# Kernel optimization log

Measured on AMD Instinct MI355X. Metric: run time of the kernel, lower is better.

Reference implementation:

```python
import jax, jax.numpy as jnp
import numpy as np

D_MODEL = 1024
N_HEADS = 16
D_HEAD = D_MODEL // N_HEADS
EPS = 1e-5
ROPE_BASE = 10000.0


def layer_norm(x, w, b=None):
    mu = jnp.mean(x, axis=-1, keepdims=True)
    var = jnp.var(x, axis=-1, keepdims=True)
    y = (x - mu) * jax.lax.rsqrt(var + EPS) * w
    return y + b if b is not None else y


def rope_cos_sin(seq_len, d_head, dtype):
    inv_freq = 1.0 / (ROPE_BASE ** (jnp.arange(0, d_head, 2, dtype=jnp.float32) / d_head))
    t = jnp.arange(seq_len, dtype=jnp.float32)
    freqs = jnp.einsum('l,f->lf', t, inv_freq)          # [L, d_head/2]
    emb = jnp.concatenate([freqs, freqs], axis=-1)       # [L, d_head]
    return jnp.cos(emb).astype(dtype), jnp.sin(emb).astype(dtype)


def rotate_half(x):
    x1, x2 = jnp.split(x, 2, axis=-1)
    return jnp.concatenate([-x2, x1], axis=-1)


def apply_rotary(x, cos, sin):
    # x: [B, L, H, Dh]; cos/sin: [L, Dh]
    c = cos[None, :, None, :]
    s = sin[None, :, None, :]
    return x * c + rotate_half(x) * s


def setup_inputs() -> dict:
    key = jax.random.key(0)
    ks = jax.random.split(key, 8)
    B, L, D = 2, 2048, D_MODEL
    x = jax.random.normal(ks[0], (B, L, D), dtype=jnp.float32)
    seq_id = jnp.sort(jax.random.randint(ks[1], (B, L), 0, 4), axis=-1).astype(jnp.int32)
    scale = 1.0 / np.sqrt(D)
    return {
        'x': x,
        'seq_id': seq_id,
        'ln1_w': jnp.ones((D,), jnp.float32),
        'ln1_b': jnp.zeros((D,), jnp.float32),
        'w_qkv': jax.random.normal(ks[2], (D, 3 * D), jnp.float32) * scale,
        'q_ln_w': jnp.ones((D,), jnp.float32),
        'k_ln_w': jnp.ones((D,), jnp.float32),
        'w_out': jax.random.normal(ks[3], (D, D), jnp.float32) * scale,
    }


def reference(x, seq_id, ln1_w, ln1_b, w_qkv, q_ln_w, k_ln_w, w_out):
    B, L, D = x.shape
    h = layer_norm(x, ln1_w, ln1_b)
    qkv = h @ w_qkv                                    # [B, L, 3D]
    q, k, v = jnp.split(qkv, 3, axis=-1)
    q = layer_norm(q, q_ln_w)                          # qk-LN over full d_model, no bias
    k = layer_norm(k, k_ln_w)
    q = q.reshape(B, L, N_HEADS, D_HEAD)
    k = k.reshape(B, L, N_HEADS, D_HEAD)
    v = v.reshape(B, L, N_HEADS, D_HEAD)
    cos, sin = rope_cos_sin(L, D_HEAD, x.dtype)
    q = apply_rotary(q, cos, sin)
    k = apply_rotary(k, cos, sin)
    scale = 1.0 / np.sqrt(D_HEAD)
    scores = jnp.einsum('bqhd,bkhd->bhqk', q, k) * scale   # [B, H, L, L]
    mask = (seq_id[:, :, None] == seq_id[:, None, :])[:, None, :, :]  # [B,1,L,L]
    scores = jnp.where(mask, scores, jnp.finfo(scores.dtype).min)
    probs = jax.nn.softmax(scores, axis=-1)
    ctx = jnp.einsum('bhqk,bkhd->bqhd', probs, v).reshape(B, L, D)
    return ctx @ w_out
```

## Files before the change

### kernel.cpp

```cpp
#include <hip/hip_runtime.h>
#include <hip/hip_bf16.h>
#include <cstdint>
#include <math.h>

#define LSEQ 2048
#define BATCH 2
#define NHEAD 16
#define DHEAD 64
#define DMODEL 1024
#define ROWS (BATCH*LSEQ)

typedef __bf16 bf16x8 __attribute__((ext_vector_type(8)));
typedef float f32x4 __attribute__((ext_vector_type(4)));
typedef unsigned short u16;

#define GLD(lds_base, src_g) \
  __builtin_amdgcn_global_load_lds((const __attribute__((address_space(1))) void*)(src_g), \
                                   (__attribute__((address_space(3))) void*)(lds_base), 16, 0, 0)
#define VM(n) asm volatile("s_waitcnt vmcnt(" #n ")" ::: "memory")

__device__ __forceinline__ u16 f2bf(float f) {
  unsigned int u = __float_as_uint(f);
  u += 0x7fffu + ((u >> 16) & 1u);
  return (u16)(u >> 16);
}
__device__ __forceinline__ float bf2f(u16 u) {
  return __uint_as_float(((unsigned)u) << 16);
}

__global__ void k_transpose_cvt(const float* __restrict__ in, u16* __restrict__ out, int R, int C) {
  __shared__ float tile[32][33];
  int c0 = blockIdx.x * 32, r0 = blockIdx.y * 32;
  int tx = threadIdx.x, ty = threadIdx.y;
#pragma unroll
  for (int i = 0; i < 32; i += 8)
    tile[ty + i][tx] = in[(size_t)(r0 + ty + i) * C + (c0 + tx)];
  __syncthreads();
#pragma unroll
  for (int i = 0; i < 32; i += 8)
    out[(size_t)(c0 + ty + i) * R + (r0 + tx)] = f2bf(tile[tx][ty + i]);
}

__global__ void k_transpose_u16(const u16* __restrict__ in, u16* __restrict__ out) {
  __shared__ u16 tile[32][33];
  int hd = blockIdx.z;
  int l0 = blockIdx.y * 32, d0 = blockIdx.x * 32;
  const u16* ip = in + (size_t)hd * LSEQ * DHEAD;
  u16* op = out + (size_t)hd * LSEQ * DHEAD;
  int tx = threadIdx.x, ty = threadIdx.y;
#pragma unroll
  for (int i = 0; i < 32; i += 8)
    tile[ty + i][tx] = ip[(size_t)(l0 + ty + i) * DHEAD + d0 + tx];
  __syncthreads();
#pragma unroll
  for (int i = 0; i < 32; i += 8)
    op[(size_t)(d0 + ty + i) * LSEQ + l0 + tx] = tile[tx][ty + i];
}

__global__ void k_rope_tables(float* __restrict__ cosb, float* __restrict__ sinb,
                              const int* __restrict__ seq, int* __restrict__ bnd) {
  if (blockIdx.x == 0 && threadIdx.x < BATCH * 5) {
    int b = threadIdx.x / 5, s = threadIdx.x % 5;
    const int* row = seq + b * LSEQ;
    int lo = 0, hi = LSEQ;
    while (lo < hi) { int mid = (lo + hi) >> 1; if (row[mid] < s) lo = mid + 1; else hi = mid; }
    bnd[b * 5 + s] = lo;
  }
  int idx = blockIdx.x * blockDim.x + threadIdx.x;
  if (idx >= LSEQ * 32) return;
  int l = idx >> 5, f = idx & 31;
  double inv = pow(10000.0, -(double)f / 32.0);
  float ang = (float)l * (float)inv;
  cosb[idx] = cosf(ang);
  sinb[idx] = sinf(ang);
}

__global__ __launch_bounds__(256) void k_ln1(const float* __restrict__ x, const float* __restrict__ w,
                                             const float* __restrict__ bias, u16* __restrict__ h) {
  int row = blockIdx.x, t = threadIdx.x;
  const float4 xv = ((const float4*)(x + (size_t)row * DMODEL))[t];
  float s = xv.x + xv.y + xv.z + xv.w;
  float s2 = xv.x * xv.x + xv.y * xv.y + xv.z * xv.z + xv.w * xv.w;
#pragma unroll
  for (int m2 = 1; m2 < 64; m2 <<= 1) { s += __shfl_xor(s, m2); s2 += __shfl_xor(s2, m2); }
  __shared__ float rb[2][4];
  int wv = t >> 6;
  if ((t & 63) == 0) { rb[0][wv] = s; rb[1][wv] = s2; }
  __syncthreads();
  s  = rb[0][0] + rb[0][1] + rb[0][2] + rb[0][3];
  s2 = rb[1][0] + rb[1][1] + rb[1][2] + rb[1][3];
  float mu = s * (1.0f / DMODEL);
  float rs = rsqrtf(s2 * (1.0f / DMODEL) - mu * mu + 1e-5f);
  const float4 wv4 = ((const float4*)w)[t];
  const float4 bv4 = ((const float4*)bias)[t];
  ushort4 o;
  o.x = f2bf((xv.x - mu) * rs * wv4.x + bv4.x);
  o.y = f2bf((xv.y - mu) * rs * wv4.y + bv4.y);
  o.z = f2bf((xv.z - mu) * rs * wv4.z + bv4.z);
  o.w = f2bf((xv.w - mu) * rs * wv4.w + bv4.w);
  ((ushort4*)(h + (size_t)row * DMODEL))[t] = o;
}

template<int OUTMODE>
__global__ __launch_bounds__(512, 2) void k_gemm256(const u16* __restrict__ A, const u16* __restrict__ B,
                                                    void* __restrict__ Cv, int M, int N, int K) {
  __shared__ __align__(16) u16 As[2][256 * 64];
  __shared__ __align__(16) u16 Bs[2][192 * 64];
  const int t = threadIdx.x, lane = t & 63, w = t >> 6;
  const int wr = w >> 2, wc = w & 3;
  const int nbx = N / 192;
  const int nwg = nbx * (M >> 8);
  const int cpx = nwg >> 3;
  const int bid = blockIdx.x;
  const int sw = (bid & 7) * cpx + (bid >> 3);
  const int m0 = (sw / nbx) * 256, n0 = (sw % nbx) * 192;
  const int NT = K >> 6;
  const int cg16 = (lane >> 4) * 16;

  f32x4 acc[8][3] = {};
  bf16x8 af_[4][2], bf_[3][2];
  const u16* Ap = A + (size_t)m0 * K;
  const u16* Bp = B + (size_t)n0 * K;
  const int rr0 = t >> 3;
  const int sz = ((t & 7) * 8) ^ ((rr0 & 7) << 3);
  const u16* pA[4] = { Ap + (size_t)rr0 * K + sz,
                       Ap + (size_t)(rr0 + 64) * K + sz,
                       Ap + (size_t)(rr0 + 128) * K + sz,
                       Ap + (size_t)(rr0 + 192) * K + sz };
  const u16* pB[3] = { Bp + (size_t)rr0 * K + sz,
                       Bp + (size_t)(rr0 + 64) * K + sz,
                       Bp + (size_t)(rr0 + 128) * K + sz };

#define SA2(b, h, EO) do { \
    GLD((char*)As + (b)*32768 + (h)*16384 + w*1024,        pA[(h)*2]     + (EO)); \
    GLD((char*)As + (b)*32768 + (h)*16384 + 8192 + w*1024, pA[(h)*2 + 1] + (EO)); \
  } while (0)
#define SB3(b, EO) do { \
    GLD((char*)Bs + (b)*24576 +         w*1024, pB[0] + (EO)); \
    GLD((char*)Bs + (b)*24576 +  8192 + w*1024, pB[1] + (EO)); \
    GLD((char*)Bs + (b)*24576 + 16384 + w*1024, pB[2] + (EO)); \
  } while (0)

#define READ_AF(asb, mh) do { \
    _Pragma("unroll") for (int i2 = 0; i2 < 4; i2++) { \
      const int rowA = (((mh)*4 + i2)*2 + wr)*16 + (lane & 15); \
      const int sA = (rowA & 7) << 4; \
      _Pragma("unroll") for (int kk = 0; kk < 2; kk++) \
        af_[i2][kk] = *(const bf16x8*)((const char*)(asb) + (rowA & 127)*128 + ((kk*64 + cg16) ^ sA)); \
    } } while (0)
#define READ_BF(bsb) do { \
    _Pragma("unroll") for (int j2 = 0; j2 < 3; j2++) { \
      const int rowB = (j2*4 + wc)*16 + (lane & 15); \
      const int sB = (rowB & 7) << 4; \
      _Pragma("unroll") for (int kk = 0; kk < 2; kk++) \
        bf_[j2][kk] = *(const bf16x8*)((const char*)(bsb) + rowB*128 + ((kk*64 + cg16) ^ sB)); \
    } } while (0)
#define MFMA24(mh) do { \
    _Pragma("unroll") for (int kk = 0; kk < 2; kk++) \
      _Pragma("unroll") for (int i2 = 0; i2 < 4; i2++) \
        _Pragma("unroll") for (int j2 = 0; j2 < 3; j2++) \
          acc[(mh)*4+i2][j2] = __builtin_amdgcn_mfma_f32_16x16x32_bf16( \
              af_[i2][kk], bf_[j2][kk], acc[(mh)*4+i2][j2], 0, 0, 0); \
  } while (0)

  SA2(0, 0, 0); SA2(0, 1, 0); SB3(0, 0);
  SA2(1, 0, 64);
  VM(2);
  __builtin_amdgcn_s_barrier();

  const char* a0  = (const char*)As;
  const char* a0h = a0 + 16384;
  const char* a1  = a0 + 32768;
  const char* a1h = a0 + 49152;
  const char* b0  = (const char*)Bs;
  const char* b1  = b0 + 24576;
  const int NIT = NT >> 1;
  for (int i = 0; i < NIT; i++) {
    const bool lst = (i == NIT - 1);
    READ_AF(a0, 0); READ_BF(b0);
    SA2(1, 1, 64); SB3(1, 64);
    __builtin_amdgcn_s_barrier();
    asm volatile("s_waitcnt lgkmcnt(0)" ::: "memory");
    __builtin_amdgcn_s_setprio(1); MFMA24(0); __builtin_amdgcn_s_setprio(0);
    __builtin_amdgcn_s_barrier();
    READ_AF(a0h, 1);
    if (!lst) SA2(0, 0, 128);
    __builtin_amdgcn_s_barrier();
    asm volatile("s_waitcnt lgkmcnt(0)" ::: "memory");
    __builtin_amdgcn_s_setprio(1); MFMA24(1); __builtin_amdgcn_s_setprio(0);
    if (lst) VM(0); else VM(2);
    __builtin_amdgcn_s_barrier();
    READ_AF(a1, 0); READ_BF(b1);
    if (!lst) { SA2(0, 1, 128); SB3(0, 128); }
    __builtin_amdgcn_s_barrier();
    asm volatile("s_waitcnt lgkmcnt(0)" ::: "memory");
    __builtin_amdgcn_s_setprio(1); MFMA24(0); __builtin_amdgcn_s_setprio(0);
    __builtin_amdgcn_s_barrier();
    READ_AF(a1h, 1);
    if (!lst) SA2(1, 0, 192);
    __builtin_amdgcn_s_barrier();
    asm volatile("s_waitcnt lgkmcnt(0)" ::: "memory");
    __builtin_amdgcn_s_setprio(1); MFMA24(1); __builtin_amdgcn_s_setprio(0);
    if (!lst) VM(2);
    __builtin_amdgcn_s_barrier();
    pA[0] += 128; pA[1] += 128; pA[2] += 128; pA[3] += 128;
    pB[0] += 128; pB[1] += 128; pB[2] += 128;
  }
#undef MFMA24
#undef READ_BF
#undef READ_AF
#undef SA2
#undef SB3

  const int cr = (lane >> 4) * 4, cc = lane & 15;
#pragma unroll
  for (int fi = 0; fi < 8; fi++)
#pragma unroll
    for (int fj = 0; fj < 3; fj++) {
      const size_t roff = (size_t)(m0 + (fi * 2 + wr) * 16 + cr) * N + (n0 + (fj * 4 + wc) * 16 + cc);
      if (OUTMODE == 0) {
        float* Cp = (float*)Cv + roff;
#pragma unroll
        for (int r = 0; r < 4; r++) Cp[(size_t)r * N] = acc[fi][fj][r];
      } else {
        u16* Cp = (u16*)Cv + roff;
#pragma unroll
        for (int r = 0; r < 4; r++) Cp[(size_t)r * N] = f2bf(acc[fi][fj][r]);
      }
    }
}

template<int OUTMODE>
__global__ __launch_bounds__(256) void k_gemm_bt(const u16* __restrict__ A, const u16* __restrict__ B,
                                                 void* __restrict__ Cv, int M, int N, int K) {
  __shared__ __align__(16) u16 As[2][128 * 64];
  __shared__ __align__(16) u16 Bs[2][128 * 64];
  const int t = threadIdx.x;
  const int lane = t & 63, w = t >> 6;
  const int nbx = N >> 7;
  const int nwg = nbx * (M >> 7);
  const int cpx = nwg >> 3;
  const int bid = blockIdx.x;
  const int sw = (bid & 7) * cpx + (bid >> 3);
  const int m0 = (sw / nbx) * 128, n0 = (sw % nbx) * 128;
  const int wm = (w >> 1) * 64, wn = (w & 1) * 64;
  const int NT = K >> 6;
  f32x4 acc[4][4] = {};
  const u16* Ap = A + (size_t)m0 * K;
  const u16* Bp = B + (size_t)n0 * K;
  const int cr0 = lane >> 3, cs = lane & 7;

#define GSTAGE(bb, kt_) do { \
    _Pragma("unroll") \
    for (int s2 = 0; s2 < 4; s2++) { \
      int ch = w * 4 + s2; \
      int row = ch * 8 + cr0; \
      int cb = cs ^ (row & 7); \
      GLD((char*)As[bb] + ch * 1024, Ap + (size_t)row * K + (kt_) * 64 + cb * 8); \
      GLD((char*)Bs[bb] + ch * 1024, Bp + (size_t)row * K + (kt_) * 64 + cb * 8); \
    } } while (0)

  GSTAGE(0, 0);
  VM(0);
  __builtin_amdgcn_s_barrier();
  int cur = 0;
  for (int kt = 0; kt < NT; kt++) {
    if (kt + 1 < NT) GSTAGE(cur ^ 1, kt + 1);
    const u16* asb = As[cur];
    const u16* bsb = Bs[cur];
#pragma unroll
    for (int kk = 0; kk < 2; kk++) {
      bf16x8 af[4], bfr[4];
#pragma unroll
      for (int i = 0; i < 4; i++) {
        int rowa = wm + i * 16 + (lane & 15);
        af[i] = *(const bf16x8*)((const char*)asb + rowa * 128 + ((kk * 64 + (lane >> 4) * 16) ^ ((rowa & 7) << 4)));
        int rowb = wn + i * 16 + (lane & 15);
        bfr[i] = *(const bf16x8*)((const char*)bsb + rowb * 128 + ((kk * 64 + (lane >> 4) * 16) ^ ((rowb & 7) << 4)));
      }
#pragma unroll
      for (int mf = 0; mf < 4; mf++)
#pragma unroll
        for (int nf = 0; nf < 4; nf++)
          acc[mf][nf] = __builtin_amdgcn_mfma_f32_16x16x32_bf16(af[mf], bfr[nf], acc[mf][nf], 0, 0, 0);
    }
    VM(0);
    __builtin_amdgcn_s_barrier();
    cur ^= 1;
  }
#undef GSTAGE
  const int cr = (lane >> 4) * 4, cc = lane & 15;
#pragma unroll
  for (int mf = 0; mf < 4; mf++)
#pragma unroll
    for (int nf = 0; nf < 4; nf++) {
      if (OUTMODE == 0) {
        float* Cp = (float*)Cv + (size_t)(m0 + wm + mf * 16 + cr) * N + (n0 + wn + nf * 16 + cc);
#pragma unroll
        for (int r = 0; r < 4; r++) Cp[(size_t)r * N] = acc[mf][nf][r];
      } else {
        u16* Cp = (u16*)Cv + (size_t)(m0 + wm + mf * 16 + cr) * N + (n0 + wn + nf * 16 + cc);
#pragma unroll
        for (int r = 0; r < 4; r++) Cp[(size_t)r * N] = f2bf(acc[mf][nf][r]);
      }
    }
}

__global__ __launch_bounds__(256) void k_qk_ln_rope(const u16* __restrict__ qkv,
                                                    const float* __restrict__ qw, const float* __restrict__ kw,
                                                    const float* __restrict__ cosb, const float* __restrict__ sinb,
                                                    u16* __restrict__ Q, u16* __restrict__ K, u16* __restrict__ V) {
  int row = blockIdx.x, t = threadIdx.x;
  int b = row >> 11, l = row & 2047;
  const u16* base = qkv + (size_t)row * 3072;
  ushort4 qu = ((const ushort4*)base)[t];
  ushort4 ku = ((const ushort4*)(base + 1024))[t];
  ushort4 vu = ((const ushort4*)(base + 2048))[t];
  float qx = bf2f(qu.x), qy = bf2f(qu.y), qz = bf2f(qu.z), qw_ = bf2f(qu.w);
  float kx = bf2f(ku.x), ky = bf2f(ku.y), kz = bf2f(ku.z), kw_ = bf2f(ku.w);
  float red[4];
  red[0] = qx + qy + qz + qw_;
  red[1] = qx * qx + qy * qy + qz * qz + qw_ * qw_;
  red[2] = kx + ky + kz + kw_;
  red[3] = kx * kx + ky * ky + kz * kz + kw_ * kw_;
#pragma unroll
  for (int i = 0; i < 4; i++)
#pragma unroll
    for (int m2 = 1; m2 < 64; m2 <<= 1) red[i] += __shfl_xor(red[i], m2);
  __shared__ float rb[4][4];
  int w = t >> 6;
  if ((t & 63) == 0) { rb[w][0] = red[0]; rb[w][1] = red[1]; rb[w][2] = red[2]; rb[w][3] = red[3]; }
  __syncthreads();
  float S1 = rb[0][0] + rb[1][0] + rb[2][0] + rb[3][0];
  float S2 = rb[0][1] + rb[1][1] + rb[2][1] + rb[3][1];
  float S3 = rb[0][2] + rb[1][2] + rb[2][2] + rb[3][2];
  float S4 = rb[0][3] + rb[1][3] + rb[2][3] + rb[3][3];
  float muq = S1 * (1.0f / DMODEL), rsq = rsqrtf(S2 * (1.0f / DMODEL) - muq * muq + 1e-5f);
  float muk = S3 * (1.0f / DMODEL), rsk = rsqrtf(S4 * (1.0f / DMODEL) - muk * muk + 1e-5f);
  __shared__ float qs[1024], ks[1024];
  float4 qwv = ((const float4*)qw)[t];
  float4 kwv = ((const float4*)kw)[t];
  qs[t * 4 + 0] = (qx - muq) * rsq * qwv.x;  ks[t * 4 + 0] = (kx - muk) * rsk * kwv.x;
  qs[t * 4 + 1] = (qy - muq) * rsq * qwv.y;  ks[t * 4 + 1] = (ky - muk) * rsk * kwv.y;
  qs[t * 4 + 2] = (qz - muq) * rsq * qwv.z;  ks[t * 4 + 2] = (kz - muk) * rsk * kwv.z;
  qs[t * 4 + 3] = (qw_ - muq) * rsq * qwv.w; ks[t * 4 + 3] = (kw_ - muk) * rsk * kwv.w;
  __syncthreads();
  int d0 = t * 4;
  int hh = d0 >> 6;
  union { ushort4 v4; u16 e[4]; } qo, ko;
#pragma unroll
  for (int i = 0; i < 4; i++) {
    int d = d0 + i, dd = d & 63, fr = dd & 31;
    float c = cosb[l * 32 + fr], s = sinb[l * 32 + fr];
    float q1 = qs[d], q2 = (dd < 32) ? -qs[d + 32] : qs[d - 32];
    float k1 = ks[d], k2 = (dd < 32) ? -ks[d + 32] : ks[d - 32];
    qo.e[i] = f2bf(q1 * c + q2 * s);
    ko.e[i] = f2bf(k1 * c + k2 * s);
  }
  size_t oidx = ((size_t)(b * NHEAD + hh) * LSEQ + l) * DHEAD + (d0 & 63);
  *(ushort4*)(Q + oidx) = qo.v4;
  *(ushort4*)(K + oidx) = ko.v4;
  *(ushort4*)(V + oidx) = vu;
}

__global__ __launch_bounds__(512) void k_attn(const u16* __restrict__ Q, const u16* __restrict__ Kb,
                                              const u16* __restrict__ VTb, const int* __restrict__ seq,
                                              const int* __restrict__ bnd, u16* __restrict__ ctx) {
  __shared__ __align__(16) u16 Ks[2][64 * 64];
  __shared__ __align__(16) u16 Vs[2][64 * 64];
  __shared__ __align__(16) u16 Pw[8][16 * 64];

  const int bid = blockIdx.x;
  const int sw = (bid & 7) * 64 + (bid >> 3);
  const int qt = sw & 15, h = (sw >> 4) & 15, b = sw >> 8;
  const int t = threadIdx.x, l = t & 63, w = t >> 6;
  const int c = l & 15, g = l >> 4;
  const int q0 = qt * 128;
  const size_t hoff = (size_t)(b * NHEAD + h) * LSEQ * DHEAD;
  const u16* Qg = Q + hoff;
  const u16* Kg = Kb + hoff;
  const u16* Vg = VTb + hoff;
  const int* seqb = seq + b * LSEQ;
  const int* bnd5 = bnd + b * 5;

  const int qw0 = q0 + w * 16;
  const int myq = qw0 + c;
  const int sq = seqb[myq];
  const int lo = bnd5[sq], hi = bnd5[sq + 1];
  const int wlo = bnd5[seqb[qw0]];
  const int whi = bnd5[seqb[qw0 + 15] + 1];
  int kbeg = bnd5[seqb[q0]] & ~63;
  int kend = (bnd5[seqb[q0 + 127] + 1] + 63) & ~63;
  if (kend > LSEQ) kend = LSEQ;

  bf16x8 qf[2];
  qf[0] = *(const bf16x8*)(Qg + (size_t)myq * 64 + g * 8);
  qf[1] = *(const bf16x8*)(Qg + (size_t)myq * 64 + 32 + g * 8);

  f32x4 acc[4] = {};
  float lsum = 0.f;

  const int rr = t >> 3;
  const int szk = ((t & 7) * 8) ^ ((rr & 7) << 3);
  const u16* pK = Kg + (size_t)rr * 64 + szk;
  const u16* pV = Vg + (size_t)rr * LSEQ + szk;

#define STAGE(bb, kt_) do { \
    GLD((char*)Ks[bb] + w * 1024, pK + (size_t)(kt_) * 64); \
    GLD((char*)Vs[bb] + w * 1024, pV + (kt_)); \
  } while (0)

  STAGE(0, kbeg);
  int cur = 0;
  for (int kt = kbeg; kt < kend; kt += 64) {
    const bool more = (kt + 64) < kend;
    if (more) STAGE(cur ^ 1, kt + 64);
    if (more) VM(2);
    else      VM(0);
    __builtin_amdgcn_s_barrier();
    __builtin_amdgcn_sched_barrier(0);
    if (kt < whi && kt + 64 > wlo) {
      const u16* ksb = Ks[cur];
      const u16* vsb = Vs[cur];
      f32x4 st[4] = {};
#pragma unroll
      for (int kk = 0; kk < 2; kk++) {
        bf16x8 kf[4];
#pragma unroll
        for (int i = 0; i < 4; i++) {
          int row = i * 16 + c;
          kf[i] = *(const bf16x8*)((const char*)ksb + row * 128 + ((kk * 64 + g * 16) ^ ((row & 7) << 4)));
        }
#pragma unroll
        for (int i = 0; i < 4; i++)
          st[i] = __builtin_amdgcn_mfma_f32_16x16x32_bf16(kf[i], qf[kk], st[i], 0, 0, 0);
      }
      const int kb0 = kt + g * 4;
#pragma unroll
      for (int i = 0; i < 4; i++) {
        float p[4];
#pragma unroll
        for (int r = 0; r < 4; r++) {
          int kglob = kb0 + i * 16 + r;
          bool ok = ((unsigned)(kglob - lo)) < ((unsigned)(hi - lo));
          float x = ok ? fmaf(st[i][r], 0.125f, -8.0f) : -1e30f;
          p[r] = __expf(x);
          lsum += p[r];
        }
        unsigned w0, w1;
        asm("v_cvt_pk_bf16_f32 %0, %1, %2" : "=v"(w0) : "v"(p[0]), "v"(p[1]));
        asm("v_cvt_pk_bf16_f32 %0, %1, %2" : "=v"(w1) : "v"(p[2]), "v"(p[3]));
        uint2 wp; wp.x = w0; wp.y = w1;
        *(uint2*)((char*)Pw[w] + c * 128 + ((i * 32 + g * 8) ^ ((c & 7) << 4))) = wp;
      }
#pragma unroll
      for (int kk = 0; kk < 2; kk++) {
        bf16x8 pa = *(const bf16x8*)((char*)Pw[w] + c * 128 + ((kk * 64 + g * 16) ^ ((c & 7) << 4)));
        bf16x8 vf[4];
#pragma unroll
        for (int df = 0; df < 4; df++) {
          int row = df * 16 + c;
          vf[df] = *(const bf16x8*)((const char*)vsb + row * 128 + ((kk * 64 + g * 16) ^ ((row & 7) << 4)));
        }
#pragma unroll
        for (int df = 0; df < 4; df++)
          acc[df] = __builtin_amdgcn_mfma_f32_16x16x32_bf16(pa, vf[df], acc[df], 0, 0, 0);
      }
    }
    __builtin_amdgcn_sched_barrier(0);
    __builtin_amdgcn_s_barrier();
    cur ^= 1;
  }
#undef STAGE

  lsum += __shfl_xor(lsum, 16);
  lsum += __shfl_xor(lsum, 32);
#pragma unroll
  for (int r = 0; r < 4; r++) {
    float lr = __shfl(lsum, g * 4 + r, 64);
    float rls = 1.0f / lr;
    int qrow = qw0 + g * 4 + r;
    u16* op = ctx + (size_t)(b * LSEQ + qrow) * DMODEL + h * 64 + c;
#pragma unroll
    for (int df = 0; df < 4; df++)
      op[df * 16] = f2bf(acc[df][r] * rls);
  }
}

extern "C" void kernel_launch(void* const* d_in, const int* in_sizes, int n_in,
                              void* d_out, int out_size, void* d_ws, size_t ws_size,
                              hipStream_t stream) {
  const float* x    = (const float*)d_in[0];
  const int*   seq  = (const int*)d_in[1];
  const float* ln1w = (const float*)d_in[2];
  const float* ln1b = (const float*)d_in[3];
  const float* wqkv = (const float*)d_in[4];
  const float* qlnw = (const float*)d_in[5];
  const float* klnw = (const float*)d_in[6];
  const float* wout = (const float*)d_in[7];
  float* out = (float*)d_out;

  char* p = (char*)d_ws;
  u16* wqkvT = (u16*)p;  p += (size_t)3072 * 1024 * 2;
  u16* woutT = (u16*)p;  p += (size_t)1024 * 1024 * 2;
  u16* hbuf  = (u16*)p;  p += (size_t)ROWS * DMODEL * 2;
  u16* Qb    = (u16*)p;  p += (size_t)ROWS * DMODEL * 2;
  u16* Kbuf  = (u16*)p;  p += (size_t)ROWS * DMODEL * 2;
  u16* Vbuf  = (u16*)p;  p += (size_t)ROWS * DMODEL * 2;
  u16* VTbuf = (u16*)p;  p += (size_t)ROWS * DMODEL * 2;
  u16* ctxb  = (u16*)p;  p += (size_t)ROWS * DMODEL * 2;
  float* cosb = (float*)p; p += (size_t)LSEQ * 32 * 4;
  float* sinb = (float*)p; p += (size_t)LSEQ * 32 * 4;
  int* bnd   = (int*)p;  p += 256;
  u16* qkv   = (u16*)p;  p += (size_t)ROWS * 3072 * 2;

  k_transpose_cvt<<<dim3(3072 / 32, 1024 / 32), dim3(32, 8), 0, stream>>>(wqkv, wqkvT, 1024, 3072);
  k_transpose_cvt<<<dim3(1024 / 32, 1024 / 32), dim3(32, 8), 0, stream>>>(wout, woutT, 1024, 1024);
  k_rope_tables<<<(LSEQ * 32) / 256, 256, 0, stream>>>(cosb, sinb, seq, bnd);
  k_ln1<<<ROWS, 256, 0, stream>>>(x, ln1w, ln1b, hbuf);
  k_gemm256<1><<<(ROWS / 256) * (3072 / 192), 512, 0, stream>>>(hbuf, wqkvT, (void*)qkv, ROWS, 3072, 1024);
  k_qk_ln_rope<<<ROWS, 256, 0, stream>>>(qkv, qlnw, klnw, cosb, sinb, Qb, Kbuf, Vbuf);
  k_transpose_u16<<<dim3(DHEAD / 32, LSEQ / 32, BATCH * NHEAD), dim3(32, 8), 0, stream>>>(Vbuf, VTbuf);
  k_attn<<<BATCH * NHEAD * (LSEQ / 128), 512, 0, stream>>>(Qb, Kbuf, VTbuf, seq, bnd, ctxb);
  k_gemm_bt<0><<<(ROWS / 128) * (1024 / 128), 256, 0, stream>>>(ctxb, woutT, (void*)out, ROWS, 1024, 1024);
}
```

Before: 123.3 us.

## Fuse prep kernels into one launch and halve QKV GEMM M-tile

Merges the weight transpose/convert, rope table, segment boundary and LN1 kernels into a single block-dispatched prep kernel, removing three launches and their serialization gaps. Separately, the QKV GEMM tile shrinks from 256x192 to 128x192 with occupancy hint raised to 4, doubling the workgroup count to 512 so more CUs are busy. Smaller M tiles increase B-operand reloads and lower per-block arithmetic intensity.

New measurement: 112.3 us. 8.9% less time.

```diff
diff --git a/kernel.cpp b/kernel.cpp
--- a/kernel.cpp
+++ b/kernel.cpp
@@ -26,19 +26,6 @@
 }
 __device__ __forceinline__ float bf2f(u16 u) {
   return __uint_as_float(((unsigned)u) << 16);
-}
-
-__global__ void k_transpose_cvt(const float* __restrict__ in, u16* __restrict__ out, int R, int C) {
-  __shared__ float tile[32][33];
-  int c0 = blockIdx.x * 32, r0 = blockIdx.y * 32;
-  int tx = threadIdx.x, ty = threadIdx.y;
-#pragma unroll
-  for (int i = 0; i < 32; i += 8)
-    tile[ty + i][tx] = in[(size_t)(r0 + ty + i) * C + (c0 + tx)];
-  __syncthreads();
-#pragma unroll
-  for (int i = 0; i < 32; i += 8)
-    out[(size_t)(c0 + ty + i) * R + (r0 + tx)] = f2bf(tile[tx][ty + i]);
 }
 
 __global__ void k_transpose_u16(const u16* __restrict__ in, u16* __restrict__ out) {
@@ -57,84 +44,99 @@
     op[(size_t)(d0 + ty + i) * LSEQ + l0 + tx] = tile[tx][ty + i];
 }
 
-__global__ void k_rope_tables(float* __restrict__ cosb, float* __restrict__ sinb,
-                              const int* __restrict__ seq, int* __restrict__ bnd) {
-  if (blockIdx.x == 0 && threadIdx.x < BATCH * 5) {
-    int b = threadIdx.x / 5, s = threadIdx.x % 5;
-    const int* row = seq + b * LSEQ;
-    int lo = 0, hi = LSEQ;
-    while (lo < hi) { int mid = (lo + hi) >> 1; if (row[mid] < s) lo = mid + 1; else hi = mid; }
-    bnd[b * 5 + s] = lo;
+__global__ __launch_bounds__(256) void k_prep(const float* __restrict__ x, const float* __restrict__ ln1w,
+                                              const float* __restrict__ ln1b, u16* __restrict__ hbuf,
+                                              const float* __restrict__ wqkv, u16* __restrict__ wqkvT,
+                                              const float* __restrict__ wout, u16* __restrict__ woutT,
+                                              const int* __restrict__ seq, int* __restrict__ bnd,
+                                              float* __restrict__ cosb, float* __restrict__ sinb) {
+  __shared__ float tile[32][33];
+  __shared__ float rb[2][4];
+  const int bid = blockIdx.x, t = threadIdx.x;
+  if (bid < 4096) {
+    const int row = bid;
+    const float4 xv = ((const float4*)(x + (size_t)row * DMODEL))[t];
+    float s = xv.x + xv.y + xv.z + xv.w;
+    float s2 = xv.x * xv.x + xv.y * xv.y + xv.z * xv.z + xv.w * xv.w;
+#pragma unroll
+    for (int m2 = 1; m2 < 64; m2 <<= 1) { s += __shfl_xor(s, m2); s2 += __shfl_xor(s2, m2); }
+    int wv = t >> 6;
+    if ((t & 63) == 0) { rb[0][wv] = s; rb[1][wv] = s2; }
+    __syncthreads();
+    s  = rb[0][0] + rb[0][1] + rb[0][2] + rb[0][3];
+    s2 = rb[1][0] + rb[1][1] + rb[1][2] + rb[1][3];
+    float mu = s * (1.0f / DMODEL);
+    float rs = rsqrtf(s2 * (1.0f / DMODEL) - mu * mu + 1e-5f);
+    const float4 wv4 = ((const float4*)ln1w)[t];
+    const float4 bv4 = ((const float4*)ln1b)[t];
+    ushort4 o;
+    o.x = f2bf((xv.x - mu) * rs * wv4.x + bv4.x);
+    o.y = f2bf((xv.y - mu) * rs * wv4.y + bv4.y);
+    o.z = f2bf((xv.z - mu) * rs * wv4.z + bv4.z);
+    o.w = f2bf((xv.w - mu) * rs * wv4.w + bv4.w);
+    ((ushort4*)(hbuf + (size_t)row * DMODEL))[t] = o;
+  } else if (bid < 4096 + 3072 + 1024) {
+    const float* in; u16* out; int R, C, bx, by;
+    if (bid < 4096 + 3072) { int rel = bid - 4096; in = wqkv; out = wqkvT; R = 1024; C = 3072; bx = rel % 96; by = rel / 96; }
+    else                   { int rel = bid - 7168; in = wout; out = woutT; R = 1024; C = 1024; bx = rel % 32; by = rel / 32; }
+    int c0 = bx * 32, r0 = by * 32;
+    int tx = t & 31, ty = t >> 5;
+#pragma unroll
+    for (int i = 0; i < 32; i += 8)
+      tile[ty + i][tx] = in[(size_t)(r0 + ty + i) * C + (c0 + tx)];
+    __syncthreads();
+#pragma unroll
+    for (int i = 0; i < 32; i += 8)
+      out[(size_t)(c0 + ty + i) * R + (r0 + tx)] = f2bf(tile[tx][ty + i]);
+  } else {
+    const int rel = bid - 8192;
+    if (rel == 0 && t < BATCH * 5) {
+      int b = t / 5, s = t % 5;
+      const int* row = seq + b * LSEQ;
+      int lo = 0, hi = LSEQ;
+      while (lo < hi) { int mid = (lo + hi) >> 1; if (row[mid] < s) lo = mid + 1; else hi = mid; }
+      bnd[b * 5 + s] = lo;
+    }
+    int idx = rel * 256 + t;
+    if (idx < LSEQ * 32) {
+      int l = idx >> 5, f = idx & 31;
+      double inv = pow(10000.0, -(double)f / 32.0);
+      float ang = (float)l * (float)inv;
+      cosb[idx] = cosf(ang);
+      sinb[idx] = sinf(ang);
+    }
   }
-  int idx = blockIdx.x * blockDim.x + threadIdx.x;
-  if (idx >= LSEQ * 32) return;
-  int l = idx >> 5, f = idx & 31;
-  double inv = pow(10000.0, -(double)f / 32.0);
-  float ang = (float)l * (float)inv;
-  cosb[idx] = cosf(ang);
-  sinb[idx] = sinf(ang);
-}
-
-__global__ __launch_bounds__(256) void k_ln1(const float* __restrict__ x, const float* __restrict__ w,
-                                             const float* __restrict__ bias, u16* __restrict__ h) {
-  int row = blockIdx.x, t = threadIdx.x;
-  const float4 xv = ((const float4*)(x + (size_t)row * DMODEL))[t];
-  float s = xv.x + xv.y + xv.z + xv.w;
-  float s2 = xv.x * xv.x + xv.y * xv.y + xv.z * xv.z + xv.w * xv.w;
-#pragma unroll
-  for (int m2 = 1; m2 < 64; m2 <<= 1) { s += __shfl_xor(s, m2); s2 += __shfl_xor(s2, m2); }
-  __shared__ float rb[2][4];
-  int wv = t >> 6;
-  if ((t & 63) == 0) { rb[0][wv] = s; rb[1][wv] = s2; }
-  __syncthreads();
-  s  = rb[0][0] + rb[0][1] + rb[0][2] + rb[0][3];
-  s2 = rb[1][0] + rb[1][1] + rb[1][2] + rb[1][3];
-  float mu = s * (1.0f / DMODEL);
-  float rs = rsqrtf(s2 * (1.0f / DMODEL) - mu * mu + 1e-5f);
-  const float4 wv4 = ((const float4*)w)[t];
-  const float4 bv4 = ((const float4*)bias)[t];
-  ushort4 o;
-  o.x = f2bf((xv.x - mu) * rs * wv4.x + bv4.x);
-  o.y = f2bf((xv.y - mu) * rs * wv4.y + bv4.y);
-  o.z = f2bf((xv.z - mu) * rs * wv4.z + bv4.z);
-  o.w = f2bf((xv.w - mu) * rs * wv4.w + bv4.w);
-  ((ushort4*)(h + (size_t)row * DMODEL))[t] = o;
 }
 
 template<int OUTMODE>
-__global__ __launch_bounds__(512, 2) void k_gemm256(const u16* __restrict__ A, const u16* __restrict__ B,
+__global__ __launch_bounds__(512, 4) void k_gemm256(const u16* __restrict__ A, const u16* __restrict__ B,
                                                     void* __restrict__ Cv, int M, int N, int K) {
-  __shared__ __align__(16) u16 As[2][256 * 64];
+  __shared__ __align__(16) u16 As[2][128 * 64];
   __shared__ __align__(16) u16 Bs[2][192 * 64];
   const int t = threadIdx.x, lane = t & 63, w = t >> 6;
   const int wr = w >> 2, wc = w & 3;
   const int nbx = N / 192;
-  const int nwg = nbx * (M >> 8);
+  const int nwg = nbx * (M >> 7);
   const int cpx = nwg >> 3;
   const int bid = blockIdx.x;
   const int sw = (bid & 7) * cpx + (bid >> 3);
-  const int m0 = (sw / nbx) * 256, n0 = (sw % nbx) * 192;
+  const int m0 = (sw / nbx) * 128, n0 = (sw % nbx) * 192;
   const int NT = K >> 6;
   const int cg16 = (lane >> 4) * 16;
 
-  f32x4 acc[8][3] = {};
-  bf16x8 af_[4][2], bf_[3][2];
+  f32x4 acc[4][3] = {};
+  bf16x8 af_[2][2], bf_[3][2];
   const u16* Ap = A + (size_t)m0 * K;
   const u16* Bp = B + (size_t)n0 * K;
   const int rr0 = t >> 3;
   const int sz = ((t & 7) * 8) ^ ((rr0 & 7) << 3);
-  const u16* pA[4] = { Ap + (size_t)rr0 * K + sz,
-                       Ap + (size_t)(rr0 + 64) * K + sz,
-                       Ap + (size_t)(rr0 + 128) * K + sz,
-                       Ap + (size_t)(rr0 + 192) * K + sz };
+  const u16* pA[2] = { Ap + (size_t)rr0 * K + sz,
+                       Ap + (size_t)(rr0 + 64) * K + sz };
   const u16* pB[3] = { Bp + (size_t)rr0 * K + sz,
                        Bp + (size_t)(rr0 + 64) * K + sz,
                        Bp + (size_t)(rr0 + 128) * K + sz };
 
-#define SA2(b, h, EO) do { \
-    GLD((char*)As + (b)*32768 + (h)*16384 + w*1024,        pA[(h)*2]     + (EO)); \
-    GLD((char*)As + (b)*32768 + (h)*16384 + 8192 + w*1024, pA[(h)*2 + 1] + (EO)); \
-  } while (0)
+#define SA1(b, h, EO) GLD((char*)As + (b)*16384 + (h)*8192 + w*1024, pA[h] + (EO))
 #define SB3(b, EO) do { \
     GLD((char*)Bs + (b)*24576 +         w*1024, pB[0] + (EO)); \
     GLD((char*)Bs + (b)*24576 +  8192 + w*1024, pB[1] + (EO)); \
@@ -142,11 +144,11 @@
   } while (0)
 
 #define READ_AF(asb, mh) do { \
-    _Pragma("unroll") for (int i2 = 0; i2 < 4; i2++) { \
-      const int rowA = (((mh)*4 + i2)*2 + wr)*16 + (lane & 15); \
+    _Pragma("unroll") for (int i2 = 0; i2 < 2; i2++) { \
+      const int rowA = (((mh)*2 + i2)*2 + wr)*16 + (lane & 15); \
       const int sA = (rowA & 7) << 4; \
       _Pragma("unroll") for (int kk = 0; kk < 2; kk++) \
-        af_[i2][kk] = *(const bf16x8*)((const char*)(asb) + (rowA & 127)*128 + ((kk*64 + cg16) ^ sA)); \
+        af_[i2][kk] = *(const bf16x8*)((const char*)(asb) + (rowA & 63)*128 + ((kk*64 + cg16) ^ sA)); \
     } } while (0)
 #define READ_BF(bsb) do { \
     _Pragma("unroll") for (int j2 = 0; j2 < 3; j2++) { \
@@ -155,66 +157,66 @@
       _Pragma("unroll") for (int kk = 0; kk < 2; kk++) \
         bf_[j2][kk] = *(const bf16x8*)((const char*)(bsb) + rowB*128 + ((kk*64 + cg16) ^ sB)); \
     } } while (0)
-#define MFMA24(mh) do { \
+#define MFMA12(mh) do { \
     _Pragma("unroll") for (int kk = 0; kk < 2; kk++) \
-      _Pragma("unroll") for (int i2 = 0; i2 < 4; i2++) \
+      _Pragma("unroll") for (int i2 = 0; i2 < 2; i2++) \
         _Pragma("unroll") for (int j2 = 0; j2 < 3; j2++) \
-          acc[(mh)*4+i2][j2] = __builtin_amdgcn_mfma_f32_16x16x32_bf16( \
-              af_[i2][kk], bf_[j2][kk], acc[(mh)*4+i2][j2], 0, 0, 0); \
+          acc[(mh)*2+i2][j2] = __builtin_amdgcn_mfma_f32_16x16x32_bf16( \
+              af_[i2][kk], bf_[j2][kk], acc[(mh)*2+i2][j2], 0, 0, 0); \
   } while (0)
 
-  SA2(0, 0, 0); SA2(0, 1, 0); SB3(0, 0);
-  SA2(1, 0, 64);
-  VM(2);
+  SA1(0, 0, 0); SA1(0, 1, 0); SB3(0, 0);
+  SA1(1, 0, 64);
+  VM(1);
   __builtin_amdgcn_s_barrier();
 
   const char* a0  = (const char*)As;
-  const char* a0h = a0 + 16384;
-  const char* a1  = a0 + 32768;
-  const char* a1h = a0 + 49152;
+  const char* a0h = a0 + 8192;
+  const char* a1  = a0 + 16384;
+  const char* a1h = a0 + 24576;
   const char* b0  = (const char*)Bs;
   const char* b1  = b0 + 24576;
   const int NIT = NT >> 1;
   for (int i = 0; i < NIT; i++) {
     const bool lst = (i == NIT - 1);
     READ_AF(a0, 0); READ_BF(b0);
-    SA2(1, 1, 64); SB3(1, 64);
+    SA1(1, 1, 64); SB3(1, 64);
     __builtin_amdgcn_s_barrier();
     asm volatile("s_waitcnt lgkmcnt(0)" ::: "memory");
-    __builtin_amdgcn_s_setprio(1); MFMA24(0); __builtin_amdgcn_s_setprio(0);
+    __builtin_amdgcn_s_setprio(1); MFMA12(0); __builtin_amdgcn_s_setprio(0);
     __builtin_amdgcn_s_barrier();
     READ_AF(a0h, 1);
-    if (!lst) SA2(0, 0, 128);
+    if (!lst) SA1(0, 0, 128);
     __builtin_amdgcn_s_barrier();
     asm volatile("s_waitcnt lgkmcnt(0)" ::: "memory");
-    __builtin_amdgcn_s_setprio(1); MFMA24(1); __builtin_amdgcn_s_setprio(0);
-    if (lst) VM(0); else VM(2);
+    __builtin_amdgcn_s_setprio(1); MFMA12(1); __builtin_amdgcn_s_setprio(0);
+    if (lst) VM(0); else VM(1);
     __builtin_amdgcn_s_barrier();
     READ_AF(a1, 0); READ_BF(b1);
-    if (!lst) { SA2(0, 1, 128); SB3(0, 128); }
+    if (!lst) { SA1(0, 1, 128); SB3(0, 128); }
     __builtin_amdgcn_s_barrier();
     asm volatile("s_waitcnt lgkmcnt(0)" ::: "memory");
-    __builtin_amdgcn_s_setprio(1); MFMA24(0); __builtin_amdgcn_s_setprio(0);
+    __builtin_amdgcn_s_setprio(1); MFMA12(0); __builtin_amdgcn_s_setprio(0);
     __builtin_amdgcn_s_barrier();
     READ_AF(a1h, 1);
-    if (!lst) SA2(1, 0, 192);
+    if (!lst) SA1(1, 0, 192);
     __builtin_amdgcn_s_barrier();
     asm volatile("s_waitcnt lgkmcnt(0)" ::: "memory");
-    __builtin_amdgcn_s_setprio(1); MFMA24(1); __builtin_amdgcn_s_setprio(0);
-    if (!lst) VM(2);
-    __builtin_amdgcn_s_barrier();
-    pA[0] += 128; pA[1] += 128; pA[2] += 128; pA[3] += 128;
+    __builtin_amdgcn_s_setprio(1); MFMA12(1); __builtin_amdgcn_s_setprio(0);
+    if (!lst) VM(1);
+    __builtin_amdgcn_s_barrier();
+    pA[0] += 128; pA[1] += 128;
     pB[0] += 128; pB[1] += 128; pB[2] += 128;
   }
-#undef MFMA24
+#undef MFMA12
 #undef READ_BF
 #undef READ_AF
-#undef SA2
+#undef SA1
 #undef SB3
 
   const int cr = (lane >> 4) * 4, cc = lane & 15;
 #pragma unroll
-  for (int fi = 0; fi < 8; fi++)
+  for (int fi = 0; fi < 4; fi++)
 #pragma unroll
     for (int fj = 0; fj < 3; fj++) {
       const size_t roff = (size_t)(m0 + (fi * 2 + wr) * 16 + cr) * N + (n0 + (fj * 4 + wc) * 16 + cc);
@@ -514,11 +516,8 @@
   int* bnd   = (int*)p;  p += 256;
   u16* qkv   = (u16*)p;  p += (size_t)ROWS * 3072 * 2;
 
-  k_transpose_cvt<<<dim3(3072 / 32, 1024 / 32), dim3(32, 8), 0, stream>>>(wqkv, wqkvT, 1024, 3072);
-  k_transpose_cvt<<<dim3(1024 / 32, 1024 / 32), dim3(32, 8), 0, stream>>>(wout, woutT, 1024, 1024);
-  k_rope_tables<<<(LSEQ * 32) / 256, 256, 0, stream>>>(cosb, sinb, seq, bnd);
-  k_ln1<<<ROWS, 256, 0, stream>>>(x, ln1w, ln1b, hbuf);
-  k_gemm256<1><<<(ROWS / 256) * (3072 / 192), 512, 0, stream>>>(hbuf, wqkvT, (void*)qkv, ROWS, 3072, 1024);
+  k_prep<<<8448, 256, 0, stream>>>(x, ln1w, ln1b, hbuf, wqkv, wqkvT, wout, woutT, seq, bnd, cosb, sinb);
+  k_gemm256<1><<<(ROWS / 128) * (3072 / 192), 512, 0, stream>>>(hbuf, wqkvT, (void*)qkv, ROWS, 3072, 1024);
   k_qk_ln_rope<<<ROWS, 256, 0, stream>>>(qkv, qlnw, klnw, cosb, sinb, Qb, Kbuf, Vbuf);
   k_transpose_u16<<<dim3(DHEAD / 32, LSEQ / 32, BATCH * NHEAD), dim3(32, 8), 0, stream>>>(Vbuf, VTbuf);
   k_attn<<<BATCH * NHEAD * (LSEQ / 128), 512, 0, stream>>>(Qb, Kbuf, VTbuf, seq, bnd, ctxb);
```
